# Performance work log

Measured on AMD Instinct MI355X. Metric: run time of the kernel, lower is better.

Reference implementation:

```python
import jax, jax.numpy as jnp
import numpy as np

NUM_ITEMS = 50000
NUM_USERS = 16384   # static number of user segments (total_user universe)
H0 = 512            # encoder_hidden_size[0]
LAT = 256           # bottleneck (encoder_hidden_size[-1] / decoder_hidden_size[0])
N = 262144          # observed interactions
NT = 262144         # target interactions


def setup_inputs() -> dict:
    key = jax.random.key(0)
    ks = jax.random.split(key, 14)

    def glorot(k, shape):
        fan_in, fan_out = shape[1], shape[0]
        lim = np.sqrt(6.0 / (fan_in + fan_out)).astype(np.float32)
        return jax.random.uniform(k, shape, jnp.float32, -lim, lim)

    return {
        "user": jax.random.randint(ks[0], (N,), 0, NUM_USERS, jnp.int32),
        "item": jax.random.randint(ks[1], (N,), 0, NUM_ITEMS, jnp.int32),
        "rating": jax.random.normal(ks[2], (N,), jnp.float32),
        "target_user": jax.random.randint(ks[3], (NT,), 0, NUM_USERS, jnp.int32),
        "target_item": jax.random.randint(ks[4], (NT,), 0, NUM_ITEMS, jnp.int32),
        "target_rating": jax.random.normal(ks[5], (NT,), jnp.float32),
        # encoder_linear: Linear(num_items, H0)
        "W_enc": glorot(ks[6], (H0, NUM_ITEMS)),
        "b_enc": jnp.zeros((H0,), jnp.float32),
        # Encoder: Linear(H0, LAT) + Tanh
        "W1": glorot(ks[7], (LAT, H0)),
        "b1": jnp.zeros((LAT,), jnp.float32),
        # Decoder: Linear(LAT, H0) + Tanh
        "W2": glorot(ks[8], (H0, LAT)),
        "b2": jnp.zeros((H0,), jnp.float32),
        # decoder_linear: Linear(H0, num_items)
        "W_dec": glorot(ks[9], (NUM_ITEMS, H0)),
        "b_dec": jnp.zeros((NUM_ITEMS,), jnp.float32),
    }


def reference(user, item, rating, target_user, target_item, target_rating,
              W_enc, b_enc, W1, b1, W2, b2, W_dec, b_dec):
    # --- encoder: gather item weight rows, scale by rating, segment-sum per user ---
    # rows: [N, H0] gather from W_enc.T ([NUM_ITEMS, H0])
    rows = W_enc.T[item] * rating[:, None]
    # per-user aggregation over the full user universe (equivalent to the
    # torch unique/sort/index_add path: users with no interactions get 0 -> tanh(bias))
    agg = jax.ops.segment_sum(rows, user, num_segments=NUM_USERS)  # [U, H0]
    x = jnp.tanh(agg + b_enc)
    # --- small dense tanh MLP encoder/decoder ---
    encoded = jnp.tanh(x @ W1.T + b1)          # [U, LAT]
    decoded = jnp.tanh(encoded @ W2.T + b2)    # [U, H0] (dropout = identity, eval mode)
    # --- decoder: gather user codes & item decoder rows, rowwise dot ---
    g = decoded[target_user]                   # [NT, H0]
    w = W_dec[target_item]                     # [NT, H0]
    pred = jnp.sum(g * w, axis=-1) + b_dec[target_item]  # [NT]
    loss = jnp.mean((pred - target_rating) ** 2)
    return pred, loss
```

## Files before the change

### kernel.cpp

```cpp
#include <hip/hip_runtime.h>
#include <hip/hip_bf16.h>
#include <math.h>

#define NUM_ITEMS 50000
#define NUM_USERS 16384
#define ITEM_BINS 65536
#define H0 512
#define LAT 256
#define FP8_SCALE 64.0f
#define FP8_INV (1.0f / 64.0f)

typedef __attribute__((ext_vector_type(8))) short short8;
typedef __attribute__((ext_vector_type(4))) float floatx4;
typedef __attribute__((ext_vector_type(2))) float vf2;

__device__ __forceinline__ unsigned short f2bf(float f) {
    union { float f; unsigned i; } u; u.f = f;
    unsigned r = u.i + 0x7fff + ((u.i >> 16) & 1);
    return (unsigned short)(r >> 16);
}
__device__ __forceinline__ float bfhi(unsigned v) {
    union { unsigned i; float f; } u; u.i = v & 0xffff0000u; return u.f;
}
__device__ __forceinline__ float bflo(unsigned v) {
    union { unsigned i; float f; } u; u.i = v << 16; return u.f;
}
__device__ __forceinline__ uint4 pack8(const float* v) {
    uint4 p;
    p.x = (unsigned)f2bf(v[0]) | ((unsigned)f2bf(v[1]) << 16);
    p.y = (unsigned)f2bf(v[2]) | ((unsigned)f2bf(v[3]) << 16);
    p.z = (unsigned)f2bf(v[4]) | ((unsigned)f2bf(v[5]) << 16);
    p.w = (unsigned)f2bf(v[6]) | ((unsigned)f2bf(v[7]) << 16);
    return p;
}
__device__ __forceinline__ unsigned pkfp8_4(float a, float b, float c, float d) {
    int v = __builtin_amdgcn_cvt_pk_fp8_f32(a, b, 0, false);
    v = __builtin_amdgcn_cvt_pk_fp8_f32(c, d, v, true);
    return (unsigned)v;
}
__device__ __forceinline__ void fp8x4_to_f32(unsigned v, float* o) {
    vf2 lo = __builtin_amdgcn_cvt_pk_f32_fp8((int)v, false);
    vf2 hi = __builtin_amdgcn_cvt_pk_f32_fp8((int)v, true);
    o[0] = lo.x; o[1] = lo.y; o[2] = hi.x; o[3] = hi.y;
}

__global__ __launch_bounds__(256) void count_kernel(const int* __restrict__ user, int* __restrict__ cntU,
                                                    const int* __restrict__ t_item, int* __restrict__ cntI,
                                                    int n, int nt) {
    int i = (blockIdx.x * blockDim.x + threadIdx.x) * 4;
    if (i + 3 < n) {
        int4 u = *(const int4*)(user + i);
        atomicAdd(&cntU[u.x], 1); atomicAdd(&cntU[u.y], 1);
        atomicAdd(&cntU[u.z], 1); atomicAdd(&cntU[u.w], 1);
    } else {
        for (int k = i; k < n; ++k) atomicAdd(&cntU[user[k]], 1);
    }
    if (i + 3 < nt) {
        int4 t = *(const int4*)(t_item + i);
        atomicAdd(&cntI[t.x], 1); atomicAdd(&cntI[t.y], 1);
        atomicAdd(&cntI[t.z], 1); atomicAdd(&cntI[t.w], 1);
    } else {
        for (int k = i; k < nt; ++k) atomicAdd(&cntI[t_item[k]], 1);
    }
}

__device__ void scan_block(const int* __restrict__ cnt, int* __restrict__ offs,
                           int* __restrict__ cursor, int per) {
    __shared__ int ssum[1024];
    int t = threadIdx.x;
    int base = t * per;
    int s = 0;
    for (int j = 0; j < per; j += 4) {
        int4 v = *(const int4*)(cnt + base + j);
        s += v.x + v.y + v.z + v.w;
    }
    ssum[t] = s;
    __syncthreads();
    for (int off = 1; off < 1024; off <<= 1) {
        int v = (t >= off) ? ssum[t - off] : 0;
        __syncthreads();
        ssum[t] += v;
        __syncthreads();
    }
    int run = (t == 0) ? 0 : ssum[t - 1];
    for (int j = 0; j < per; j += 4) {
        int4 v = *(const int4*)(cnt + base + j);
        int4 o;
        o.x = run; run += v.x;
        o.y = run; run += v.y;
        o.z = run; run += v.z;
        o.w = run; run += v.w;
        *(int4*)(offs + base + j) = o;
        *(int4*)(cursor + base + j) = o;
    }
}

__global__ void scan_kernel(const int* __restrict__ cntU, int* __restrict__ offsU, int* __restrict__ curU,
                            const int* __restrict__ cntI, int* __restrict__ offsI, int* __restrict__ curI) {
    if (blockIdx.x == 0) scan_block(cntU, offsU, curU, NUM_USERS / 1024);
    else scan_block(cntI, offsI, curI, ITEM_BINS / 1024);
}

__global__ __launch_bounds__(256) void mega_kernel(
        const int* __restrict__ user, const int* __restrict__ item,
        const float* __restrict__ rating, int* __restrict__ curU, int2* __restrict__ s_pack,
        const int* __restrict__ t_user, const int* __restrict__ t_item,
        const float* __restrict__ t_rating, int* __restrict__ curI, int4* __restrict__ st_pack,
        const float* __restrict__ W_enc, unsigned char* __restrict__ wtb8,
        const float* __restrict__ W_dec, unsigned char* __restrict__ wdb8,
        const float* __restrict__ W1, unsigned short* __restrict__ w1b,
        const float* __restrict__ W2, unsigned short* __restrict__ w2b,
        int n, int nt, int SB, int TB, int DB) {
    __shared__ float tileT[64 * 129];
    int bid = blockIdx.x;
    int tid = threadIdx.x;
    if (bid < SB) {
        int i = bid * 256 + tid;
        if (i < n) {
            int u = user[i];
            int pos = atomicAdd(&curU[u], 1);
            s_pack[pos] = make_int2(item[i], __float_as_int(rating[i]));
        }
        if (i < nt) {
            int it = t_item[i];
            int pos = atomicAdd(&curI[it], 1);
            st_pack[pos] = make_int4(t_user[i], it, __float_as_int(t_rating[i]), i);
        }
    } else if (bid < SB + TB) {
        const int TBX = (NUM_ITEMS + 63) / 64;
        int b = bid - SB;
        int x0 = (b % TBX) * 64;
        int y0 = (b / TBX) * 128;
        int g = tid >> 4;
        int m = tid & 15;
        int ibase = m * 4;
#pragma unroll
        for (int p = 0; p < 8; ++p) {
            int hloc = p * 16 + g;
            int it = x0 + ibase;
            if (it < NUM_ITEMS) {
                float4 v = *(const float4*)(W_enc + (size_t)(y0 + hloc) * NUM_ITEMS + it);
                tileT[(ibase + 0) * 129 + hloc] = v.x;
                tileT[(ibase + 1) * 129 + hloc] = v.y;
                tileT[(ibase + 2) * 129 + hloc] = v.z;
                tileT[(ibase + 3) * 129 + hloc] = v.w;
            }
        }
        __syncthreads();
        int l = tid & 7;
        int i0 = tid >> 3;
#pragma unroll
        for (int p = 0; p < 2; ++p) {
            int i = p * 32 + i0;
            int it = x0 + i;
            if (it < NUM_ITEMS) {
                const float* src = tileT + i * 129 + l * 16;
                uint4 o;
                o.x = pkfp8_4(src[0] * FP8_SCALE, src[1] * FP8_SCALE, src[2] * FP8_SCALE, src[3] * FP8_SCALE);
                o.y = pkfp8_4(src[4] * FP8_SCALE, src[5] * FP8_SCALE, src[6] * FP8_SCALE, src[7] * FP8_SCALE);
                o.z = pkfp8_4(src[8] * FP8_SCALE, src[9] * FP8_SCALE, src[10] * FP8_SCALE, src[11] * FP8_SCALE);
                o.w = pkfp8_4(src[12] * FP8_SCALE, src[13] * FP8_SCALE, src[14] * FP8_SCALE, src[15] * FP8_SCALE);
                *(uint4*)(wtb8 + (size_t)it * H0 + y0 + l * 16) = o;
            }
        }
    } else if (bid < SB + TB + DB) {
        size_t idx = (size_t)(bid - SB - TB) * 4096 + tid * 16;
        float4 v0 = *(const float4*)(W_dec + idx);
        float4 v1 = *(const float4*)(W_dec + idx + 4);
        float4 v2 = *(const float4*)(W_dec + idx + 8);
        float4 v3 = *(const float4*)(W_dec + idx + 12);
        uint4 o;
        o.x = pkfp8_4(v0.x * FP8_SCALE, v0.y * FP8_SCALE, v0.z * FP8_SCALE, v0.w * FP8_SCALE);
        o.y = pkfp8_4(v1.x * FP8_SCALE, v1.y * FP8_SCALE, v1.z * FP8_SCALE, v1.w * FP8_SCALE);
        o.z = pkfp8_4(v2.x * FP8_SCALE, v2.y * FP8_SCALE, v2.z * FP8_SCALE, v2.w * FP8_SCALE);
        o.w = pkfp8_4(v3.x * FP8_SCALE, v3.y * FP8_SCALE, v3.z * FP8_SCALE, v3.w * FP8_SCALE);
        *(uint4*)(wdb8 + idx) = o;
    } else {
        int b2i = bid - SB - TB - DB;
        const float* src = (b2i < 64) ? W1 : W2;
        unsigned short* dst = (b2i < 64) ? w1b : w2b;
        int idx = (b2i & 63) * 2048 + tid * 8;
        float v[8];
        *(float4*)&v[0] = *(const float4*)(src + idx);
        *(float4*)&v[4] = *(const float4*)(src + idx + 4);
        *(uint4*)(dst + idx) = pack8(v);
    }
}

__global__ __launch_bounds__(256) void agg_kernel(const unsigned char* __restrict__ wtb8,
                                                  const int* __restrict__ offs,
                                                  const int* __restrict__ ends,
                                                  const int2* __restrict__ s_pack,
                                                  const float* __restrict__ b_enc,
                                                  unsigned short* __restrict__ xb) {
    __shared__ float red[3 * 512];
    int u = blockIdx.x;
    int tid = threadIdx.x;
    int g = tid >> 6, lane = tid & 63;
    float acc[8] = {};
    int j0 = offs[u], j1 = ends[u];
    int j = j0 + g;
    int2 nxt = (j < j1) ? s_pack[j] : make_int2(0, 0);
    while (j < j1) {
        int2 cur = nxt;
        int jn = j + 4;
        if (jn < j1) nxt = s_pack[jn];
        float r = __int_as_float(cur.y);
        uint2 v = ((const uint2*)(wtb8 + (size_t)cur.x * H0))[lane];
        float wf[8];
        fp8x4_to_f32(v.x, wf);
        fp8x4_to_f32(v.y, wf + 4);
#pragma unroll
        for (int e = 0; e < 8; ++e) acc[e] += wf[e] * r;
        j = jn;
    }
    if (g) {
        float4* rp = (float4*)red + (size_t)(g - 1) * 128 + lane * 2;
        rp[0] = make_float4(acc[0], acc[1], acc[2], acc[3]);
        rp[1] = make_float4(acc[4], acc[5], acc[6], acc[7]);
    }
    __syncthreads();
    if (g == 0) {
#pragma unroll
        for (int h = 0; h < 3; ++h) {
            const float* rp = red + h * 512 + lane * 8;
#pragma unroll
            for (int e = 0; e < 8; ++e) acc[e] += rp[e];
        }
        float4 b0 = ((const float4*)b_enc)[lane * 2];
        float4 b1 = ((const float4*)b_enc)[lane * 2 + 1];
        float o[8];
        o[0] = tanhf(acc[0] * FP8_INV + b0.x); o[1] = tanhf(acc[1] * FP8_INV + b0.y);
        o[2] = tanhf(acc[2] * FP8_INV + b0.z); o[3] = tanhf(acc[3] * FP8_INV + b0.w);
        o[4] = tanhf(acc[4] * FP8_INV + b1.x); o[5] = tanhf(acc[5] * FP8_INV + b1.y);
        o[6] = tanhf(acc[6] * FP8_INV + b1.z); o[7] = tanhf(acc[7] * FP8_INV + b1.w);
        ((uint4*)(xb + (size_t)u * H0))[lane] = pack8(o);
    }
}

template<int BN>
__global__ __launch_bounds__(256) void gemm_mfma(const unsigned short* __restrict__ A,
                                                 const unsigned short* __restrict__ B,
                                                 const float* __restrict__ bias,
                                                 unsigned short* __restrict__ C,
                                                 int Nn, int K) {
    constexpr int WN = BN / 32;
    constexpr int NCH = 8 + BN / 16;
    constexpr int PER = NCH / 4;
    __shared__ unsigned short Ash[128 * 32];
    __shared__ unsigned short Bsh[BN * 32];
    int tid = threadIdx.x;
    int wid = tid >> 6, lane = tid & 63;
    int wave_m = wid & 1, wave_n = wid >> 1;
    int quad = lane >> 4, l16 = lane & 15;
    int m0 = blockIdx.x * 128, n0 = blockIdx.y * BN;
    floatx4 acc[4][WN] = {};
    int srow = lane >> 2;
    int scol = (lane & 3) * 8;
    for (int k0 = 0; k0 < K; k0 += 32) {
#pragma unroll
        for (int i = 0; i < PER; ++i) {
            int c = wid * PER + i;
            if (c < 8) {
                const unsigned short* ga = A + (size_t)(m0 + c * 16 + srow) * K + k0 + scol;
                __builtin_amdgcn_global_load_lds(
                    (const __attribute__((address_space(1))) void*)ga,
                    (__attribute__((address_space(3))) void*)((__attribute__((address_space(3))) char*)Ash + c * 1024),
                    16, 0, 0);
            } else {
                const unsigned short* gb = B + (size_t)(n0 + (c - 8) * 16 + srow) * K + k0 + scol;
                __builtin_amdgcn_global_load_lds(
                    (const __attribute__((address_space(1))) void*)gb,
                    (__attribute__((address_space(3))) void*)((__attribute__((address_space(3))) char*)Bsh + (c - 8) * 1024),
                    16, 0, 0);
            }
        }
        __syncthreads();
        short8 af[4], bfr[WN];
#pragma unroll
        for (int i = 0; i < 4; ++i) {
            int ml = wave_m * 64 + i * 16 + l16;
            af[i] = ((const short8*)Ash)[ml * 4 + quad];
        }
#pragma unroll
        for (int j = 0; j < WN; ++j) {
            int nl = wave_n * (BN / 2) + j * 16 + l16;
            bfr[j] = ((const short8*)Bsh)[nl * 4 + quad];
        }
#pragma unroll
        for (int i = 0; i < 4; ++i)
#pragma unroll
            for (int j = 0; j < WN; ++j)
                acc[i][j] = __builtin_amdgcn_mfma_f32_16x16x32_bf16(af[i], bfr[j], acc[i][j], 0, 0, 0);
        __syncthreads();
    }
#pragma unroll
    for (int j = 0; j < WN; ++j) {
        int col = n0 + wave_n * (BN / 2) + j * 16 + l16;
        float bv = bias[col];
#pragma unroll
        for (int i = 0; i < 4; ++i) {
            int rowb = m0 + wave_m * 64 + i * 16 + quad * 4;
#pragma unroll
            for (int r = 0; r < 4; ++r)
                C[(size_t)(rowb + r) * Nn + col] = f2bf(tanhf(acc[i][j][r] + bv));
        }
    }
}

__global__ __launch_bounds__(256) void predict_kernel(const unsigned short* __restrict__ dec_b,
                                                      const unsigned char* __restrict__ wdb8,
                                                      const float* __restrict__ b_dec,
                                                      const int4* __restrict__ st,
                                                      float* __restrict__ pred,
                                                      float* __restrict__ partials, int NT) {
    __shared__ float wsum[4];
    int wid = threadIdx.x >> 6, lane = threadIdx.x & 63;
    int base = (blockIdx.x * 4 + wid) * 4;
    float sq = 0.f;
    int4 tv[4];
    uint4 gv[4];
    uint2 wv[4];
#pragma unroll
    for (int t = 0; t < 4; ++t) tv[t] = st[min(base + t, NT - 1)];
#pragma unroll
    for (int t = 0; t < 4; ++t) {
        gv[t] = ((const uint4*)(dec_b + (size_t)tv[t].x * H0))[lane];
        wv[t] = ((const uint2*)(wdb8 + (size_t)tv[t].y * H0))[lane];
    }
#pragma unroll
    for (int t = 0; t < 4; ++t) {
        float wf[8];
        fp8x4_to_f32(wv[t].x, wf);
        fp8x4_to_f32(wv[t].y, wf + 4);
        float s = bflo(gv[t].x) * wf[0] + bfhi(gv[t].x) * wf[1]
                + bflo(gv[t].y) * wf[2] + bfhi(gv[t].y) * wf[3]
                + bflo(gv[t].z) * wf[4] + bfhi(gv[t].z) * wf[5]
                + bflo(gv[t].w) * wf[6] + bfhi(gv[t].w) * wf[7];
#pragma unroll
        for (int off = 32; off; off >>= 1) s += __shfl_xor(s, off, 64);
        if (lane == 0 && base + t < NT) {
            float p = s * FP8_INV + b_dec[tv[t].y];
            pred[tv[t].w] = p;
            float d = p - __int_as_float(tv[t].z);
            sq += d * d;
        }
    }
    if (lane == 0) wsum[wid] = sq;
    __syncthreads();
    if (threadIdx.x == 0) partials[blockIdx.x] = wsum[0] + wsum[1] + wsum[2] + wsum[3];
}

__global__ void loss_reduce(const float* __restrict__ partials, float* __restrict__ out_loss,
                            int nPart, float invNT) {
    __shared__ float s[256];
    int t = threadIdx.x;
    float a = 0.f;
    const float4* p4 = (const float4*)partials;
    int n4 = nPart >> 2;
    for (int i = t; i < n4; i += 256) {
        float4 v = p4[i];
        a += v.x + v.y + v.z + v.w;
    }
    for (int i = (n4 << 2) + t; i < nPart; i += 256) a += partials[i];
    s[t] = a;
    __syncthreads();
    for (int off = 128; off; off >>= 1) {
        if (t < off) s[t] += s[t + off];
        __syncthreads();
    }
    if (t == 0) out_loss[0] = s[0] * invNT;
}

extern "C" void kernel_launch(void* const* d_in, const int* in_sizes, int n_in,
                              void* d_out, int out_size, void* d_ws, size_t ws_size,
                              hipStream_t stream) {
    const int* user = (const int*)d_in[0];
    const int* item = (const int*)d_in[1];
    const float* rating = (const float*)d_in[2];
    const int* t_user = (const int*)d_in[3];
    const int* t_item = (const int*)d_in[4];
    const float* t_rating = (const float*)d_in[5];
    const float* W_enc = (const float*)d_in[6];
    const float* b_enc = (const float*)d_in[7];
    const float* W1 = (const float*)d_in[8];
    const float* b1 = (const float*)d_in[9];
    const float* W2 = (const float*)d_in[10];
    const float* b2 = (const float*)d_in[11];
    const float* W_dec = (const float*)d_in[12];
    const float* b_dec = (const float*)d_in[13];
    const int N = in_sizes[0];
    const int NT = in_sizes[3];

    char* ws = (char*)d_ws;
    size_t off = 0;
    auto alloc = [&](size_t bytes) {
        void* p = ws + off;
        off = (off + bytes + 255) & ~(size_t)255;
        return p;
    };
    unsigned char* wtb8 = (unsigned char*)alloc((size_t)NUM_ITEMS * H0);
    unsigned char* wdb8 = (unsigned char*)alloc((size_t)NUM_ITEMS * H0);
    unsigned short* xb = (unsigned short*)alloc((size_t)NUM_USERS * H0 * 2);
    unsigned short* enc_b = (unsigned short*)alloc((size_t)NUM_USERS * LAT * 2);
    unsigned short* dec_b = (unsigned short*)alloc((size_t)NUM_USERS * H0 * 2);
    unsigned short* w1b = (unsigned short*)alloc((size_t)LAT * H0 * 2);
    unsigned short* w2b = (unsigned short*)alloc((size_t)H0 * LAT * 2);
    int* cntU = (int*)alloc((size_t)(NUM_USERS + ITEM_BINS) * 4);
    int* cntI = cntU + NUM_USERS;
    int* offsU = (int*)alloc((size_t)NUM_USERS * 4);
    int* curU = (int*)alloc((size_t)NUM_USERS * 4);
    int* offsI = (int*)alloc((size_t)ITEM_BINS * 4);
    int* curI = (int*)alloc((size_t)ITEM_BINS * 4);
    int2* s_pack = (int2*)alloc((size_t)N * 8);
    int4* st_pack = (int4*)alloc((size_t)NT * 16);
    const int predBlocks = (NT + 15) / 16;
    float* partials = (float*)alloc((size_t)predBlocks * 4);

    float* pred = (float*)d_out;
    float* loss = pred + NT;

    const int maxNNT = N > NT ? N : NT;
    const int SB = (maxNNT + 255) / 256;
    const int TBX = (NUM_ITEMS + 63) / 64;
    const int TB = TBX * (H0 / 128);
    const int DB = (NUM_ITEMS * H0) / 4096;
    const int WB = 128;

    hipMemsetAsync(cntU, 0, (size_t)(NUM_USERS + ITEM_BINS) * 4, stream);
    count_kernel<<<(maxNNT + 1023) / 1024, 256, 0, stream>>>(user, cntU, t_item, cntI, N, NT);
    scan_kernel<<<2, 1024, 0, stream>>>(cntU, offsU, curU, cntI, offsI, curI);
    mega_kernel<<<SB + TB + DB + WB, 256, 0, stream>>>(
        user, item, rating, curU, s_pack,
        t_user, t_item, t_rating, curI, st_pack,
        W_enc, wtb8, W_dec, wdb8, W1, w1b, W2, w2b,
        N, NT, SB, TB, DB);
    agg_kernel<<<NUM_USERS, 256, 0, stream>>>(wtb8, offsU, curU, s_pack, b_enc, xb);
    gemm_mfma<64><<<dim3(NUM_USERS / 128, LAT / 64), 256, 0, stream>>>(xb, w1b, b1, enc_b, LAT, H0);
    gemm_mfma<64><<<dim3(NUM_USERS / 128, H0 / 64), 256, 0, stream>>>(enc_b, w2b, b2, dec_b, H0, LAT);
    predict_kernel<<<predBlocks, 256, 0, stream>>>(dec_b, wdb8, b_dec, st_pack, pred, partials, NT);
    loss_reduce<<<1, 256, 0, stream>>>(partials, loss, predBlocks, 1.0f / NT);
}
```

Measured before the change: 454.0 us.

## Drop W_dec fp8 pre-conversion, read fp32 directly in predict, fuse loss reduction

Removes the pass that converts all of W_dec to fp8. The predict kernel now gathers fp32 W_dec rows directly, which drops a full read and write of W_dec in exchange for gathering about 4x more bytes per target row. The W_enc transpose tile is reshaped to 64x64 with vectorized shared-memory stores. The separate loss_reduce kernel is replaced by a per-block atomicAdd into a zeroed loss, removing one launch and the partials buffer but making the summation order nondeterministic.

Result: slower. 579.4 us (+27.6%).

```diff
diff --git a/kernel.cpp b/kernel.cpp
--- a/kernel.cpp
+++ b/kernel.cpp
@@ -107,11 +107,10 @@
         const int* __restrict__ t_user, const int* __restrict__ t_item,
         const float* __restrict__ t_rating, int* __restrict__ curI, int4* __restrict__ st_pack,
         const float* __restrict__ W_enc, unsigned char* __restrict__ wtb8,
-        const float* __restrict__ W_dec, unsigned char* __restrict__ wdb8,
         const float* __restrict__ W1, unsigned short* __restrict__ w1b,
         const float* __restrict__ W2, unsigned short* __restrict__ w2b,
-        int n, int nt, int SB, int TB, int DB) {
-    __shared__ float tileT[64 * 129];
+        int n, int nt, int SB, int TB) {
+    __shared__ float tileh[64 * 64];
     int bid = blockIdx.x;
     int tid = threadIdx.x;
     if (bid < SB) {
@@ -130,53 +129,33 @@
         const int TBX = (NUM_ITEMS + 63) / 64;
         int b = bid - SB;
         int x0 = (b % TBX) * 64;
-        int y0 = (b / TBX) * 128;
+        int y0 = (b / TBX) * 64;
         int g = tid >> 4;
         int m = tid & 15;
-        int ibase = m * 4;
-#pragma unroll
-        for (int p = 0; p < 8; ++p) {
+        int it4 = x0 + m * 4;
+#pragma unroll
+        for (int p = 0; p < 4; ++p) {
             int hloc = p * 16 + g;
-            int it = x0 + ibase;
-            if (it < NUM_ITEMS) {
-                float4 v = *(const float4*)(W_enc + (size_t)(y0 + hloc) * NUM_ITEMS + it);
-                tileT[(ibase + 0) * 129 + hloc] = v.x;
-                tileT[(ibase + 1) * 129 + hloc] = v.y;
-                tileT[(ibase + 2) * 129 + hloc] = v.z;
-                tileT[(ibase + 3) * 129 + hloc] = v.w;
+            if (it4 < NUM_ITEMS) {
+                float4 v = *(const float4*)(W_enc + (size_t)(y0 + hloc) * NUM_ITEMS + it4);
+                *(float4*)(tileh + hloc * 64 + m * 4) = v;
             }
         }
         __syncthreads();
-        int l = tid & 7;
-        int i0 = tid >> 3;
-#pragma unroll
-        for (int p = 0; p < 2; ++p) {
-            int i = p * 32 + i0;
-            int it = x0 + i;
-            if (it < NUM_ITEMS) {
-                const float* src = tileT + i * 129 + l * 16;
-                uint4 o;
-                o.x = pkfp8_4(src[0] * FP8_SCALE, src[1] * FP8_SCALE, src[2] * FP8_SCALE, src[3] * FP8_SCALE);
-                o.y = pkfp8_4(src[4] * FP8_SCALE, src[5] * FP8_SCALE, src[6] * FP8_SCALE, src[7] * FP8_SCALE);
-                o.z = pkfp8_4(src[8] * FP8_SCALE, src[9] * FP8_SCALE, src[10] * FP8_SCALE, src[11] * FP8_SCALE);
-                o.w = pkfp8_4(src[12] * FP8_SCALE, src[13] * FP8_SCALE, src[14] * FP8_SCALE, src[15] * FP8_SCALE);
-                *(uint4*)(wtb8 + (size_t)it * H0 + y0 + l * 16) = o;
-            }
-        }
-    } else if (bid < SB + TB + DB) {
-        size_t idx = (size_t)(bid - SB - TB) * 4096 + tid * 16;
-        float4 v0 = *(const float4*)(W_dec + idx);
-        float4 v1 = *(const float4*)(W_dec + idx + 4);
-        float4 v2 = *(const float4*)(W_dec + idx + 8);
-        float4 v3 = *(const float4*)(W_dec + idx + 12);
-        uint4 o;
-        o.x = pkfp8_4(v0.x * FP8_SCALE, v0.y * FP8_SCALE, v0.z * FP8_SCALE, v0.w * FP8_SCALE);
-        o.y = pkfp8_4(v1.x * FP8_SCALE, v1.y * FP8_SCALE, v1.z * FP8_SCALE, v1.w * FP8_SCALE);
-        o.z = pkfp8_4(v2.x * FP8_SCALE, v2.y * FP8_SCALE, v2.z * FP8_SCALE, v2.w * FP8_SCALE);
-        o.w = pkfp8_4(v3.x * FP8_SCALE, v3.y * FP8_SCALE, v3.z * FP8_SCALE, v3.w * FP8_SCALE);
-        *(uint4*)(wdb8 + idx) = o;
+        int i = tid >> 2;
+        int l = tid & 3;
+        int it = x0 + i;
+        if (it < NUM_ITEMS) {
+            const float* src = tileh + (l * 16) * 64 + i;
+            uint4 o;
+            o.x = pkfp8_4(src[0] * FP8_SCALE, src[64] * FP8_SCALE, src[128] * FP8_SCALE, src[192] * FP8_SCALE);
+            o.y = pkfp8_4(src[256] * FP8_SCALE, src[320] * FP8_SCALE, src[384] * FP8_SCALE, src[448] * FP8_SCALE);
+            o.z = pkfp8_4(src[512] * FP8_SCALE, src[576] * FP8_SCALE, src[640] * FP8_SCALE, src[704] * FP8_SCALE);
+            o.w = pkfp8_4(src[768] * FP8_SCALE, src[832] * FP8_SCALE, src[896] * FP8_SCALE, src[960] * FP8_SCALE);
+            *(uint4*)(wtb8 + (size_t)it * H0 + y0 + l * 16) = o;
+        }
     } else {
-        int b2i = bid - SB - TB - DB;
+        int b2i = bid - SB - TB;
         const float* src = (b2i < 64) ? W1 : W2;
         unsigned short* dst = (b2i < 64) ? w1b : w2b;
         int idx = (b2i & 63) * 2048 + tid * 8;
@@ -309,38 +288,38 @@
 }
 
 __global__ __launch_bounds__(256) void predict_kernel(const unsigned short* __restrict__ dec_b,
-                                                      const unsigned char* __restrict__ wdb8,
+                                                      const float* __restrict__ W_dec,
                                                       const float* __restrict__ b_dec,
                                                       const int4* __restrict__ st,
                                                       float* __restrict__ pred,
-                                                      float* __restrict__ partials, int NT) {
+                                                      float* __restrict__ loss,
+                                                      int NT, float invNT) {
     __shared__ float wsum[4];
     int wid = threadIdx.x >> 6, lane = threadIdx.x & 63;
     int base = (blockIdx.x * 4 + wid) * 4;
     float sq = 0.f;
     int4 tv[4];
     uint4 gv[4];
-    uint2 wv[4];
+    float4 w0[4], w1[4];
 #pragma unroll
     for (int t = 0; t < 4; ++t) tv[t] = st[min(base + t, NT - 1)];
 #pragma unroll
     for (int t = 0; t < 4; ++t) {
         gv[t] = ((const uint4*)(dec_b + (size_t)tv[t].x * H0))[lane];
-        wv[t] = ((const uint2*)(wdb8 + (size_t)tv[t].y * H0))[lane];
+        const float4* wp = (const float4*)(W_dec + (size_t)tv[t].y * H0);
+        w0[t] = wp[lane * 2];
+        w1[t] = wp[lane * 2 + 1];
     }
 #pragma unroll
     for (int t = 0; t < 4; ++t) {
-        float wf[8];
-        fp8x4_to_f32(wv[t].x, wf);
-        fp8x4_to_f32(wv[t].y, wf + 4);
-        float s = bflo(gv[t].x) * wf[0] + bfhi(gv[t].x) * wf[1]
-                + bflo(gv[t].y) * wf[2] + bfhi(gv[t].y) * wf[3]
-                + bflo(gv[t].z) * wf[4] + bfhi(gv[t].z) * wf[5]
-                + bflo(gv[t].w) * wf[6] + bfhi(gv[t].w) * wf[7];
+        float s = bflo(gv[t].x) * w0[t].x + bfhi(gv[t].x) * w0[t].y
+                + bflo(gv[t].y) * w0[t].z + bfhi(gv[t].y) * w0[t].w
+                + bflo(gv[t].z) * w1[t].x + bfhi(gv[t].z) * w1[t].y
+                + bflo(gv[t].w) * w1[t].z + bfhi(gv[t].w) * w1[t].w;
 #pragma unroll
         for (int off = 32; off; off >>= 1) s += __shfl_xor(s, off, 64);
         if (lane == 0 && base + t < NT) {
-            float p = s * FP8_INV + b_dec[tv[t].y];
+            float p = s + b_dec[tv[t].y];
             pred[tv[t].w] = p;
             float d = p - __int_as_float(tv[t].z);
             sq += d * d;
@@ -348,28 +327,8 @@
     }
     if (lane == 0) wsum[wid] = sq;
     __syncthreads();
-    if (threadIdx.x == 0) partials[blockIdx.x] = wsum[0] + wsum[1] + wsum[2] + wsum[3];
-}
-
-__global__ void loss_reduce(const float* __restrict__ partials, float* __restrict__ out_loss,
-                            int nPart, float invNT) {
-    __shared__ float s[256];
-    int t = threadIdx.x;
-    float a = 0.f;
-    const float4* p4 = (const float4*)partials;
-    int n4 = nPart >> 2;
-    for (int i = t; i < n4; i += 256) {
-        float4 v = p4[i];
-        a += v.x + v.y + v.z + v.w;
-    }
-    for (int i = (n4 << 2) + t; i < nPart; i += 256) a += partials[i];
-    s[t] = a;
-    __syncthreads();
-    for (int off = 128; off; off >>= 1) {
-        if (t < off) s[t] += s[t + off];
-        __syncthreads();
-    }
-    if (t == 0) out_loss[0] = s[0] * invNT;
+    if (threadIdx.x == 0)
+        atomicAdd(loss, (wsum[0] + wsum[1] + wsum[2] + wsum[3]) * invNT);
 }
 
 extern "C" void kernel_launch(void* const* d_in, const int* in_sizes, int n_in,
@@ -400,7 +359,6 @@
         return p;
     };
     unsigned char* wtb8 = (unsigned char*)alloc((size_t)NUM_ITEMS * H0);
-    unsigned char* wdb8 = (unsigned char*)alloc((size_t)NUM_ITEMS * H0);
     unsigned short* xb = (unsigned short*)alloc((size_t)NUM_USERS * H0 * 2);
     unsigned short* enc_b = (unsigned short*)alloc((size_t)NUM_USERS * LAT * 2);
     unsigned short* dec_b = (unsigned short*)alloc((size_t)NUM_USERS * H0 * 2);
@@ -414,8 +372,6 @@
     int* curI = (int*)alloc((size_t)ITEM_BINS * 4);
     int2* s_pack = (int2*)alloc((size_t)N * 8);
     int4* st_pack = (int4*)alloc((size_t)NT * 16);
-    const int predBlocks = (NT + 15) / 16;
-    float* partials = (float*)alloc((size_t)predBlocks * 4);
 
     float* pred = (float*)d_out;
     float* loss = pred + NT;
@@ -423,21 +379,21 @@
     const int maxNNT = N > NT ? N : NT;
     const int SB = (maxNNT + 255) / 256;
     const int TBX = (NUM_ITEMS + 63) / 64;
-    const int TB = TBX * (H0 / 128);
-    const int DB = (NUM_ITEMS * H0) / 4096;
+    const int TB = TBX * (H0 / 64);
     const int WB = 128;
+    const int predBlocks = (NT + 15) / 16;
 
     hipMemsetAsync(cntU, 0, (size_t)(NUM_USERS + ITEM_BINS) * 4, stream);
+    hipMemsetAsync(loss, 0, 4, stream);
     count_kernel<<<(maxNNT + 1023) / 1024, 256, 0, stream>>>(user, cntU, t_item, cntI, N, NT);
     scan_kernel<<<2, 1024, 0, stream>>>(cntU, offsU, curU, cntI, offsI, curI);
-    mega_kernel<<<SB + TB + DB + WB, 256, 0, stream>>>(
+    mega_kernel<<<SB + TB + WB, 256, 0, stream>>>(
         user, item, rating, curU, s_pack,
         t_user, t_item, t_rating, curI, st_pack,
-        W_enc, wtb8, W_dec, wdb8, W1, w1b, W2, w2b,
-        N, NT, SB, TB, DB);
+        W_enc, wtb8, W1, w1b, W2, w2b,
+        N, NT, SB, TB);
     agg_kernel<<<NUM_USERS, 256, 0, stream>>>(wtb8, offsU, curU, s_pack, b_enc, xb);
     gemm_mfma<64><<<dim3(NUM_USERS / 128, LAT / 64), 256, 0, stream>>>(xb, w1b, b1, enc_b, LAT, H0);
     gemm_mfma<64><<<dim3(NUM_USERS / 128, H0 / 64), 256, 0, stream>>>(enc_b, w2b, b2, dec_b, H0, LAT);
-    predict_kernel<<<predBlocks, 256, 0, stream>>>(dec_b, wdb8, b_dec, st_pack, pred, partials, NT);
-    loss_reduce<<<1, 256, 0, stream>>>(partials, loss, predBlocks, 1.0f / NT);
-}
+    predict_kernel<<<predBlocks, 256, 0, stream>>>(dec_b, W_dec, b_dec, st_pack, pred, loss, NT, 1.0f / NT);
+}
```
